# Kernel optimization log

Hardware: AMD Instinct MI355X
Metric: run time of the kernel (lower is better)

Reference implementation:

```python
import jax, jax.numpy as jnp
import numpy as np

P = 16          # patch_len
EPS = 1e-5      # BatchNorm eps


def _dct_mats(L):
    # torch_dct DCT-II matrices. Do: norm='ortho' (orthonormal). D2: norm=None (2*cos).
    n = np.arange(L)
    C = np.cos(np.pi * (n[None, :] + 0.5) * n[:, None] / L)
    s = np.full(L, np.sqrt(2.0 / L)); s[0] = np.sqrt(1.0 / L)
    Do = (s[:, None] * C).astype(np.float32)
    D2 = (2.0 * C).astype(np.float32)
    S = np.full(L, 1.0 / np.sqrt(2.0 * L)); S[0] = 1.0 / (2.0 * np.sqrt(L))
    return jnp.asarray(Do), jnp.asarray(D2), jnp.asarray(S.astype(np.float32))


def _gelu(t):
    return jax.nn.gelu(t, approximate=False)


def _bn(x, g, b, ch_axis=1):
    # training-mode BatchNorm1d: biased batch stats over all axes except channel
    axes = tuple(i for i in range(x.ndim) if i != ch_axis)
    m = x.mean(axes, keepdims=True)
    v = ((x - m) ** 2).mean(axes, keepdims=True)
    shp = [1] * x.ndim; shp[ch_axis] = x.shape[ch_axis]
    return (x - m) / jnp.sqrt(v + EPS) * g.reshape(shp) + b.reshape(shp)


def _quantile(a, q):
    # torch.quantile default 'linear' interpolation over flattened tensor
    s = jnp.sort(a)
    n = a.shape[0]
    pos = q * (n - 1)
    lo = jnp.clip(jnp.floor(pos).astype(jnp.int32), 0, n - 1)
    hi = jnp.clip(lo + 1, 0, n - 1)
    frac = pos - lo.astype(pos.dtype)
    return s[lo] * (1.0 - frac) + s[hi] * frac


def _topk_freq(x, Do5, wf, bf, g, b, wc, bc):
    # TopKFreq: first 5 ortho-DCT coeffs per var (torch detaches via cpu/numpy round trip)
    low = jax.lax.stop_gradient(jnp.einsum('bdl,kl->bdk', x, Do5))  # [B,D,5]
    att = jnp.einsum('bdk,k->bd', low, wf) + bf                      # conv1d k=5 stride=5
    m = att.mean(); v = ((att - m) ** 2).mean()                      # BatchNorm1d(1)
    att = (att - m) / jnp.sqrt(v + EPS) * g + b
    att = _gelu(att)
    a = jax.nn.sigmoid(att * wc + bc)                                # 1x1 conv + sigmoid
    return a[:, :, None]  # [B,D,1]; att1 == att2 (same conv used twice)


def _forward(x, dctconv_w, dctconv_b, dctnorm_g, dctnorm_b, threshold,
             embed_W, embed_b, linres_W, linres_b, depth1_w, depth1_b,
             depthnorm_g, depthnorm_b, tf_fc_w, tf_fc_b, tf_norm_g, tf_norm_b,
             tf_conv_w, tf_conv_b, mlp_w1, mlp_b1, mlp_w2, mlp_b2,
             mlpnorm_g, mlpnorm_b):
    B, L, D = x.shape
    N = L // P
    Do, D2, S = _dct_mats(L)
    dctconv = lambda t: t * dctconv_w[None, :, None] + dctconv_b[None, :, None]

    xp = x.transpose(0, 2, 1)                      # [B,D,L]
    x_res = dctconv(xp)
    z_dct = xp @ D2.T                              # dct, norm=None

    # adaptive high-freq mask (rows of 0/1 per (b,d))
    energy = (z_dct ** 2).sum(-1)                  # [B,D]
    med = jnp.median(energy, axis=1, keepdims=True)
    ne = energy / (med + 1e-6)
    thr = _quantile(ne.ravel(), threshold[0])
    mask = (ne > thr).astype(x.dtype)[:, :, None]

    z = dctconv(z_dct * mask)
    z = _gelu(z)
    z = _bn(z, dctnorm_g, dctnorm_b)
    z1 = (z * S) @ Do + x_res                      # idct(norm=None)

    # non-overlapping patching (stride == patch_len)
    zp = xp.reshape(B * D, N, P)
    ze = jnp.einsum('bnp,dp->bnd', zp, embed_W) + embed_b    # [BD,N,3P]
    z_res = ze.reshape(B, D, N * 3 * P) @ linres_W.T + linres_b  # [B,D,pred]

    zr = ze.reshape(B * D, N, P, 3)                # depthwise conv k=3 stride=3
    z1r = jnp.einsum('bnpj,nj->bnp', zr, depth1_w) + depth1_b[None, :, None]
    zd = _gelu(_bn(z1r, depthnorm_g, depthnorm_b))
    z2 = zd.reshape(B, D, L)

    tf = lambda t: _topk_freq(t, Do[:5], tf_fc_w, tf_fc_b[0], tf_norm_g[0],
                              tf_norm_b[0], tf_conv_w[0], tf_conv_b[0])
    att = tf(z1 + z2)
    z1 = z1 * att
    z2 = z2 * att
    z = z1 + z2
    z_att = tf(z)
    z = _gelu(_bn(z, dctnorm_g, dctnorm_b))
    inter = _gelu(_bn(dctconv(z), dctnorm_g, dctnorm_b)) * z_att
    z1 = z1 * inter + z2
    z2 = z2 * inter + z1                           # uses updated z1
    z = z1 * z2 + z1 + z2
    z = _gelu(_bn(z, dctnorm_g, dctnorm_b))

    # Mlp: fc1 applied twice (identical), gelu gate, BN over vars channel, fc2
    h = z @ mlp_w1.T + mlp_b1                      # [B,D,pred//2]
    h = _gelu(h) * h
    h = _bn(h, mlpnorm_g, mlpnorm_b)
    z_mlp = h @ mlp_w2.T + mlp_b2 + z_res          # [B,D,pred]
    return z_mlp.transpose(0, 2, 1)                # [B,pred,D]


def setup_inputs():
    key = jax.random.key(0)
    ks = jax.random.split(key, 14)
    B, L, D, PRED = 2048, 512, 7, 96
    N, DM, H = L // P, 3 * P, PRED // 2
    f32 = jnp.float32
    rn = lambda k, shape, s: jax.random.normal(k, shape, dtype=f32) * s
    return {
        'x': jax.random.normal(ks[0], (B, L, D), dtype=f32),
        'dctconv_w': rn(ks[1], (D,), 0.5),
        'dctconv_b': rn(ks[2], (D,), 0.02),
        'dctnorm_g': jnp.ones((D,), f32),
        'dctnorm_b': jnp.zeros((D,), f32),
        'threshold': jax.random.uniform(ks[3], (1,), dtype=f32) * 0.5,
        'embed_W': rn(ks[4], (DM, P), 0.1),
        'embed_b': rn(ks[5], (DM,), 0.02),
        'linres_W': rn(ks[6], (PRED, N * DM), 0.02),
        'linres_b': rn(ks[7], (PRED,), 0.02),
        'depth1_w': rn(ks[8], (N, 3), 0.3),
        'depth1_b': rn(ks[9], (N,), 0.02),
        'depthnorm_g': jnp.ones((N,), f32),
        'depthnorm_b': jnp.zeros((N,), f32),
        'tf_fc_w': rn(ks[10], (5,), 0.3),
        'tf_fc_b': rn(ks[10], (1,), 0.02),
        'tf_norm_g': jnp.ones((1,), f32),
        'tf_norm_b': jnp.zeros((1,), f32),
        'tf_conv_w': rn(ks[11], (1,), 0.5),
        'tf_conv_b': rn(ks[11], (1,), 0.02),
        'mlp_w1': rn(ks[12], (H, L), 0.04),
        'mlp_b1': rn(ks[12], (H,), 0.02),
        'mlp_w2': rn(ks[13], (PRED, H), 0.1),
        'mlp_b2': rn(ks[13], (PRED,), 0.02),
        'mlpnorm_g': jnp.ones((D,), f32),
        'mlpnorm_b': jnp.zeros((D,), f32),
    }


def reference(x, dctconv_w, dctconv_b, dctnorm_g, dctnorm_b, threshold,
              embed_W, embed_b, linres_W, linres_b, depth1_w, depth1_b,
              depthnorm_g, depthnorm_b, tf_fc_w, tf_fc_b, tf_norm_g, tf_norm_b,
              tf_conv_w, tf_conv_b, mlp_w1, mlp_b1, mlp_w2, mlp_b2,
              mlpnorm_g, mlpnorm_b):
    return _forward(x, dctconv_w, dctconv_b, dctnorm_g, dctnorm_b, threshold,
                    embed_W, embed_b, linres_W, linres_b, depth1_w, depth1_b,
                    depthnorm_g, depthnorm_b, tf_fc_w, tf_fc_b, tf_norm_g,
                    tf_norm_b, tf_conv_w, tf_conv_b, mlp_w1, mlp_b1, mlp_w2,
                    mlp_b2, mlpnorm_g, mlpnorm_b)
```

## Files before the change

kernel.cpp:

```cpp
#include <hip/hip_runtime.h>
#include <math.h>

#define BB 2048
#define LL 512
#define DD 7
#define BD 14336

constexpr size_t F_XP   = 0;
constexpr size_t F_ZG   = F_XP  + (size_t)BD*512;
constexpr size_t F_Z1   = F_ZG  + (size_t)BD*512;
constexpr size_t F_CLK  = F_Z1  + (size_t)BD*512;
constexpr size_t F_MKL  = F_CLK + 512*512;
constexpr size_t F_U    = F_MKL + 512*512;
constexpr size_t F_CSUM = F_U + 512;
constexpr size_t F_W2   = F_CSUM + 512;
constexpr size_t F_CST  = F_W2 + 96*512;
constexpr size_t F_V    = F_CST + 96;
constexpr size_t F_C2   = F_V + 32*256;
constexpr size_t F_ZRES = F_C2 + 512;
constexpr size_t F_H2   = F_ZRES + (size_t)BD*96;
constexpr size_t F_EN   = F_H2 + (size_t)BD*48;
constexpr size_t F_NE   = F_EN + BD;
constexpr size_t F_ATT  = F_NE + BD;
constexpr size_t F_A1   = F_ATT + BD;
constexpr size_t F_A2   = F_A1 + BD;
constexpr size_t F_RS   = F_A2 + BD;
constexpr size_t F_RQ   = F_RS + BD;
constexpr size_t F_PS   = F_RQ + BD;
constexpr size_t F_PQ   = F_PS + 1792*32;
constexpr size_t F_BN   = F_PQ + 1792*32;
constexpr size_t F_THR  = F_BN + 256;

typedef __attribute__((ext_vector_type(8))) short bf8;
typedef __attribute__((ext_vector_type(4))) float f4;

__device__ __forceinline__ float gelu_f(float x) {
  return 0.5f * x * (1.0f + erff(x * 0.70710678118654752440f));
}
__device__ __forceinline__ float sigm_f(float x) {
  return 1.0f / (1.0f + expf(-x));
}
__device__ __forceinline__ float wred(float v) {
#pragma unroll
  for (int o = 32; o > 0; o >>= 1) v += __shfl_down(v, o);
  return v;
}
__device__ __forceinline__ unsigned bfh_u(float v) {
  unsigned u = __float_as_uint(v);
  return (u + 0x7FFFu + ((u >> 16) & 1u)) >> 16;
}
__device__ __forceinline__ float bf2f(unsigned h) { return __uint_as_float(h << 16); }

__global__ void k_gen_b(ushort* __restrict__ B1H, ushort* __restrict__ B1L,
                        ushort* __restrict__ B2H, ushort* __restrict__ B2L) {
  int c = blockIdx.x;
  for (int r = threadIdx.x; r < 512; r += 256) {
    double c1 = cos(3.14159265358979323846 * (r + 0.5) * c / 512.0);
    float v1 = (float)(2.0 * c1);
    unsigned h = bfh_u(v1);
    B1H[(size_t)c*512 + r] = (ushort)h;
    B1L[(size_t)c*512 + r] = (ushort)bfh_u(v1 - bf2f(h));
    double c2 = cos(3.14159265358979323846 * (c + 0.5) * r / 512.0);
    float v2 = (float)(c2 * (r == 0 ? (1.0/1024.0) : (1.0/512.0)));
    h = bfh_u(v2);
    B2H[(size_t)c*512 + r] = (ushort)h;
    B2L[(size_t)c*512 + r] = (ushort)bfh_u(v2 - bf2f(h));
  }
}

__global__ void k_ucsum2(float* __restrict__ u, float* __restrict__ csum,
                         const float* __restrict__ wf) {
  int l = blockIdx.x*256 + threadIdx.x;
  if (l >= 512) return;
  double th2 = 3.14159265358979323846 * (double)(2*l + 1) / 2048.0;
  double s = (l & 1) ? -1.0 : 1.0;
  double S = 0.5*s/tan(th2) - 0.5;
  csum[l] = (float)(1.0/1024.0 + S/512.0);
  double uu = (double)wf[0] * 45.25483399593904156 / 1024.0;
  for (int k = 1; k < 5; ++k)
    uu += (double)wf[k] * 32.0 * cos(3.14159265358979323846*(l+0.5)*k/512.0) / 512.0;
  u[l] = (float)uu;
}

__global__ __launch_bounds__(256) void k_w2(const float* __restrict__ linW,
    const float* __restrict__ linb, const float* __restrict__ eW, const float* __restrict__ eb,
    ushort* __restrict__ W2H, ushort* __restrict__ W2L, float* __restrict__ cst)
{
  __shared__ float sW[768];
  __shared__ float sb[48];
  __shared__ float rbuf[256];
  int o = blockIdx.x, t = threadIdx.x;
  for (int i = t; i < 768; i += 256) sW[i] = eW[i];
  if (t < 48) sb[t] = eb[t];
  __syncthreads();
  const float* lw = linW + (size_t)o * 1536;
  for (int i = t; i < 512; i += 256) {
    int n = i >> 4, p = i & 15;
    float s = 0.f;
    const float* l2 = lw + n*48;
#pragma unroll 8
    for (int m = 0; m < 48; ++m) s += l2[m] * sW[m*16 + p];
    unsigned hb = bfh_u(s);
    W2H[(size_t)o*512 + i] = (ushort)hb;
    W2L[(size_t)o*512 + i] = (ushort)bfh_u(s - bf2f(hb));
  }
  float c = 0.f;
  for (int i = t; i < 1536; i += 256) c += lw[i] * sb[i % 48];
  rbuf[t] = c; __syncthreads();
  for (int off = 128; off > 0; off >>= 1) { if (t < off) rbuf[t] += rbuf[t+off]; __syncthreads(); }
  if (t == 0) cst[o] = rbuf[0] + linb[o];
}

__global__ void k_splitw(const float* __restrict__ src, ushort* __restrict__ H,
                         ushort* __restrict__ L, int n) {
  int i = blockIdx.x*256 + threadIdx.x;
  if (i < n) {
    float v = src[i];
    unsigned hb = bfh_u(v);
    H[i] = (ushort)hb;
    L[i] = (ushort)bfh_u(v - bf2f(hb));
  }
}

__global__ void k_v(const float* __restrict__ eW, const float* __restrict__ eb,
                    const float* __restrict__ dw, const float* __restrict__ db,
                    float* __restrict__ V, float* __restrict__ c2)
{
  int n = blockIdx.x, t = threadIdx.x;
  int p = t >> 4, q = t & 15;
  float s = 0.f;
#pragma unroll
  for (int j = 0; j < 3; ++j) s += eW[(p*3+j)*16 + q] * dw[n*3+j];
  V[(size_t)n*256 + p*16 + q] = s;
  if (q == 0) {
    float c = 0.f;
#pragma unroll
    for (int j = 0; j < 3; ++j) c += eb[p*3+j] * dw[n*3+j];
    c2[n*16+p] = c + db[n];
  }
}

__global__ __launch_bounds__(256) void k_transpose(const float* __restrict__ x, float* __restrict__ xp) {
  __shared__ float s[3584];
  int b = blockIdx.x;
  const float* src = x + (size_t)b*3584;
  for (int c = threadIdx.x; c < 896; c += 256) {
    float4 v = *(const float4*)&src[c*4];
    s[c*4+0]=v.x; s[c*4+1]=v.y; s[c*4+2]=v.z; s[c*4+3]=v.w;
  }
  __syncthreads();
  for (int c = threadIdx.x; c < 896; c += 256) {
    int d = c >> 7, cg = c & 127;
    float4 v;
    v.x = s[(cg*4+0)*7 + d]; v.y = s[(cg*4+1)*7 + d];
    v.z = s[(cg*4+2)*7 + d]; v.w = s[(cg*4+3)*7 + d];
    *(float4*)&xp[((size_t)b*7 + d)*512 + cg*4] = v;
  }
}

template<int MODE>
__global__ __launch_bounds__(256) void k_mfma(
    const float* __restrict__ Af32,
    const ushort* __restrict__ AHg, const ushort* __restrict__ ALg,
    const ushort* __restrict__ BHg, const ushort* __restrict__ BLg,
    float* __restrict__ z1out, ushort* __restrict__ GH, ushort* __restrict__ GL,
    const float* __restrict__ bnac, const float* __restrict__ csum,
    const float* __restrict__ xp,
    const float* __restrict__ cw, const float* __restrict__ cb,
    const float* __restrict__ ne, const float* __restrict__ thr,
    float* __restrict__ rs, float* __restrict__ rq)
{
  __shared__ ushort AhS[64*40], AlS[64*40];
  __shared__ ushort BhS[256*40], BlS[256*40];
  const int t = threadIdx.x;
  const int lane = t & 63, w = t >> 6;
  const int l15 = lane & 15, l4 = lane >> 4;
  const int r0 = blockIdx.x * 64, c0 = blockIdx.y * 256;

  f4 acc[4][4];
#pragma unroll
  for (int i = 0; i < 4; ++i)
#pragma unroll
    for (int j = 0; j < 4; ++j) acc[i][j] = (f4){0.f,0.f,0.f,0.f};

  const int arow = t >> 2, ak0 = (t & 3) * 8;

  for (int kt = 0; kt < 512; kt += 32) {
    if (MODE == 2) {
      const float* src = Af32 + (size_t)(r0+arow)*512 + kt + ak0;
      float4 v0 = *(const float4*)src;
      float4 v1 = *(const float4*)(src+4);
      float va[8] = {v0.x,v0.y,v0.z,v0.w,v1.x,v1.y,v1.z,v1.w};
      bf8 hv, lv;
#pragma unroll
      for (int j = 0; j < 8; ++j) {
        unsigned hb = bfh_u(va[j]);
        hv[j] = (short)hb;
        lv[j] = (short)bfh_u(va[j] - bf2f(hb));
      }
      *(bf8*)&AhS[arow*40 + ak0] = hv;
      *(bf8*)&AlS[arow*40 + ak0] = lv;
    } else {
      *(bf8*)&AhS[arow*40 + ak0] = *(const bf8*)&AHg[(size_t)(r0+arow)*512 + kt + ak0];
      *(bf8*)&AlS[arow*40 + ak0] = *(const bf8*)&ALg[(size_t)(r0+arow)*512 + kt + ak0];
    }
#pragma unroll
    for (int h = 0; h < 4; ++h) {
      int c = t + h*256;
      int brow = c >> 2, bk0 = (c & 3) * 8;
      *(bf8*)&BhS[brow*40 + bk0] = *(const bf8*)&BHg[(size_t)(c0+brow)*512 + kt + bk0];
      *(bf8*)&BlS[brow*40 + bk0] = *(const bf8*)&BLg[(size_t)(c0+brow)*512 + kt + bk0];
    }
    __syncthreads();
    bf8 ah[4], al[4], bh[4], bl[4];
#pragma unroll
    for (int fr = 0; fr < 4; ++fr) {
      int off = (fr*16 + l15)*40 + l4*8;
      ah[fr] = *(const bf8*)&AhS[off];
      al[fr] = *(const bf8*)&AlS[off];
    }
#pragma unroll
    for (int fc = 0; fc < 4; ++fc) {
      int off = (w*64 + fc*16 + l15)*40 + l4*8;
      bh[fc] = *(const bf8*)&BhS[off];
      bl[fc] = *(const bf8*)&BlS[off];
    }
#pragma unroll
    for (int fr = 0; fr < 4; ++fr)
#pragma unroll
      for (int fc = 0; fc < 4; ++fc) {
        acc[fr][fc] = __builtin_amdgcn_mfma_f32_16x16x32_bf16(ah[fr], bh[fc], acc[fr][fc], 0, 0, 0);
        acc[fr][fc] = __builtin_amdgcn_mfma_f32_16x16x32_bf16(ah[fr], bl[fc], acc[fr][fc], 0, 0, 0);
        acc[fr][fc] = __builtin_amdgcn_mfma_f32_16x16x32_bf16(al[fr], bh[fc], acc[fr][fc], 0, 0, 0);
      }
    __syncthreads();
  }

  const float thv = (MODE == 2) ? thr[0] : 0.f;
#pragma unroll
  for (int fr = 0; fr < 4; ++fr)
#pragma unroll
    for (int j = 0; j < 4; ++j) {
      const int r = r0 + fr*16 + l4*4 + j;
      const int d = r % 7;
      if (MODE == 1) {
        const float aR = bnac[d], cR = bnac[7+d], wv = cw[d], bvv = cb[d];
#pragma unroll
        for (int fc = 0; fc < 4; ++fc) {
          int col = c0 + w*64 + fc*16 + l15;
          float val = acc[fr][fc][j];
          z1out[(size_t)r*512 + col] = aR*val + cR*csum[col] + xp[(size_t)r*512 + col]*wv + bvv;
        }
      } else {
        float m = (ne[r] > thv) ? 1.0f : 0.0f;
        float wm = cw[d] * m, bvv = cb[d];
        float s = 0.f, q = 0.f;
#pragma unroll
        for (int fc = 0; fc < 4; ++fc) {
          int col = c0 + w*64 + fc*16 + l15;
          float g = gelu_f(acc[fr][fc][j]*wm + bvv);
          unsigned hb = bfh_u(g);
          GH[(size_t)r*512 + col] = (ushort)hb;
          GL[(size_t)r*512 + col] = (ushort)bfh_u(g - bf2f(hb));
          s += g; q += g*g;
        }
#pragma unroll
        for (int off = 8; off > 0; off >>= 1) {
          s += __shfl_down(s, off, 16);
          q += __shfl_down(q, off, 16);
        }
        if (l15 == 0) { atomicAdd(&rs[r], s); atomicAdd(&rq[r], q); }
      }
    }
}

template<int NCOLS, int MODE>
__global__ __launch_bounds__(256) void k_mfma_nt(
    const float* __restrict__ Af32,
    const ushort* __restrict__ WH, const ushort* __restrict__ WL,
    const float* __restrict__ bias, float* __restrict__ outp,
    const float* __restrict__ ta, const float* __restrict__ tc,
    float* __restrict__ rs, float* __restrict__ rq)
{
  constexpr int NF = NCOLS / 16;
  __shared__ ushort AhS[64*40], AlS[64*40];
  __shared__ ushort BhS[NCOLS*40], BlS[NCOLS*40];
  const int t = threadIdx.x;
  const int lane = t & 63, w = t >> 6;
  const int l15 = lane & 15, l4 = lane >> 4;
  const int r0 = blockIdx.x * 64;

  f4 acc[NF];
#pragma unroll
  for (int fc = 0; fc < NF; ++fc) acc[fc] = (f4){0.f,0.f,0.f,0.f};

  const int arow = t >> 2, ak0 = (t & 3) * 8;
  float taa = 0.f, tcc = 0.f;
  if (MODE == 1) { int d = (r0 + arow) % 7; taa = ta[d]; tcc = tc[d]; }

  for (int kt = 0; kt < 512; kt += 32) {
    {
      const float* src = Af32 + (size_t)(r0+arow)*512 + kt + ak0;
      float4 v0 = *(const float4*)src;
      float4 v1 = *(const float4*)(src+4);
      float va[8] = {v0.x,v0.y,v0.z,v0.w,v1.x,v1.y,v1.z,v1.w};
      bf8 hv, lv;
#pragma unroll
      for (int j = 0; j < 8; ++j) {
        float x = va[j];
        if (MODE == 1) x = gelu_f(taa*x + tcc);
        unsigned hb = bfh_u(x);
        hv[j] = (short)hb;
        lv[j] = (short)bfh_u(x - bf2f(hb));
      }
      *(bf8*)&AhS[arow*40 + ak0] = hv;
      *(bf8*)&AlS[arow*40 + ak0] = lv;
    }
    for (int c = t; c < NCOLS*4; c += 256) {
      int brow = c >> 2, bk0 = (c & 3) * 8;
      *(bf8*)&BhS[brow*40 + bk0] = *(const bf8*)&WH[(size_t)brow*512 + kt + bk0];
      *(bf8*)&BlS[brow*40 + bk0] = *(const bf8*)&WL[(size_t)brow*512 + kt + bk0];
    }
    __syncthreads();
    bf8 ah, al;
    {
      int off = (w*16 + l15)*40 + l4*8;
      ah = *(const bf8*)&AhS[off];
      al = *(const bf8*)&AlS[off];
    }
#pragma unroll
    for (int fc = 0; fc < NF; ++fc) {
      int off = (fc*16 + l15)*40 + l4*8;
      bf8 bh = *(const bf8*)&BhS[off];
      bf8 bl = *(const bf8*)&BlS[off];
      acc[fc] = __builtin_amdgcn_mfma_f32_16x16x32_bf16(ah, bh, acc[fc], 0, 0, 0);
      acc[fc] = __builtin_amdgcn_mfma_f32_16x16x32_bf16(ah, bl, acc[fc], 0, 0, 0);
      acc[fc] = __builtin_amdgcn_mfma_f32_16x16x32_bf16(al, bh, acc[fc], 0, 0, 0);
    }
    __syncthreads();
  }

#pragma unroll
  for (int j = 0; j < 4; ++j) {
    const int r = r0 + w*16 + l4*4 + j;
    float s = 0.f, q = 0.f;
#pragma unroll
    for (int fc = 0; fc < NF; ++fc) {
      int col = fc*16 + l15;
      float v = acc[fc][j] + bias[col];
      if (MODE == 1) { float g = gelu_f(v); v = g*v; }
      outp[(size_t)r*NCOLS + col] = v;
      if (MODE == 1) { s += v; q += v*v; }
    }
    if (MODE == 1) {
#pragma unroll
      for (int off = 8; off > 0; off >>= 1) {
        s += __shfl_down(s, off, 16);
        q += __shfl_down(q, off, 16);
      }
      if (l15 == 0) { rs[r] = s; rq[r] = q; }
    }
  }
}

__global__ void k_energy_an(const float* __restrict__ xp, float* __restrict__ en) {
  int r = blockIdx.x*4 + (threadIdx.x >> 6);
  int lane = threadIdx.x & 63;
  const float* row = xp + (size_t)r*512;
  double s = 0.0, q = 0.0;
  for (int i = lane; i < 512; i += 64) { double v = row[i]; s += v; q += v*v; }
#pragma unroll
  for (int o = 32; o > 0; o >>= 1) { s += __shfl_down(s, o); q += __shfl_down(q, o); }
  if (lane == 0) en[r] = (float)(1024.0*q + 2.0*s*s);
}

__global__ void k_ne(const float* __restrict__ en, float* __restrict__ ne) {
  int b = blockIdx.x*256 + threadIdx.x;
  if (b >= 2048) return;
  float e[7], s7[7];
#pragma unroll
  for (int d = 0; d < 7; ++d) { e[d] = en[b*7+d]; s7[d] = e[d]; }
#pragma unroll
  for (int i = 1; i < 7; ++i) {
    float key = s7[i]; int j = i-1;
    while (j >= 0 && s7[j] > key) { s7[j+1] = s7[j]; --j; }
    s7[j+1] = key;
  }
  float med = s7[3] + 1e-6f;
#pragma unroll
  for (int d = 0; d < 7; ++d) ne[b*7+d] = e[d] / med;
}

__global__ __launch_bounds__(1024) void k_thr(const float* __restrict__ ne,
                                              const float* __restrict__ qp, float* __restrict__ out)
{
  __shared__ unsigned s_part[16][8];
  __shared__ unsigned s_bsel, s_R;
  const int t = threadIdx.x;
  const int lane = t & 63, wv = t >> 6;
  unsigned key[14];
#pragma unroll
  for (int j = 0; j < 14; ++j) key[j] = __float_as_uint(ne[t + j*1024]);

  float q = qp[0];
  float pos = q * 14335.0f;
  int lo = (int)floorf(pos);
  if (lo < 0) lo = 0; if (lo > 14335) lo = 14335;
  int hi = lo + 1; if (hi > 14335) hi = 14335;
  float frac = pos - (float)lo;

  unsigned prefix = 0;
  unsigned R = (unsigned)lo;
#pragma unroll 1
  for (int shift = 28; shift >= 0; shift -= 4) {
    unsigned pb = prefix >> shift;
    unsigned long long accb = 0ull;
#pragma unroll
    for (int j = 0; j < 14; ++j) {
      unsigned diff = (key[j] >> shift) - pb;
      accb += (diff < 16u) ? (1ull << (diff*4)) : 0ull;
    }
    unsigned pk[8];
#pragma unroll
    for (int b = 0; b < 8; ++b) {
      unsigned clo = (unsigned)(accb >> (b*4)) & 15u;
      unsigned chi = (unsigned)(accb >> (b*4+32)) & 15u;
      pk[b] = clo | (chi << 16);
    }
#pragma unroll
    for (int b = 0; b < 8; ++b)
#pragma unroll
      for (int o = 32; o > 0; o >>= 1) pk[b] += __shfl_down(pk[b], o);
    if (lane == 0) {
#pragma unroll
      for (int b = 0; b < 8; ++b) s_part[wv][b] = pk[b];
    }
    __syncthreads();
    if (t == 0) {
      unsigned tot[16];
#pragma unroll
      for (int i = 0; i < 8; ++i) {
        unsigned s = 0;
#pragma unroll
        for (int w2 = 0; w2 < 16; ++w2) s += s_part[w2][i];
        tot[i] = s & 0xFFFFu; tot[i+8] = s >> 16;
      }
      unsigned cum = 0, bsel = 15;
#pragma unroll 1
      for (int b = 0; b < 16; ++b) {
        if (cum + tot[b] > R) { bsel = (unsigned)b; break; }
        cum += tot[b];
      }
      s_bsel = bsel; s_R = R - cum;
    }
    __syncthreads();
    prefix |= (s_bsel << shift);
    R = s_R;
    __syncthreads();
  }
  unsigned cle = 0, mn = 0xFFFFFFFFu;
#pragma unroll
  for (int j = 0; j < 14; ++j) {
    cle += (key[j] <= prefix) ? 1u : 0u;
    if (key[j] > prefix && key[j] < mn) mn = key[j];
  }
#pragma unroll
  for (int o = 32; o > 0; o >>= 1) {
    cle += __shfl_down(cle, o);
    unsigned m2 = __shfl_down(mn, o);
    mn = (m2 < mn) ? m2 : mn;
  }
  if (lane == 0) { s_part[wv][0] = cle; s_part[wv][1] = mn; }
  __syncthreads();
  if (t == 0) {
    unsigned C = 0, M = 0xFFFFFFFFu;
#pragma unroll
    for (int w2 = 0; w2 < 16; ++w2) {
      C += s_part[w2][0];
      if (s_part[w2][1] < M) M = s_part[w2][1];
    }
    unsigned vhiKey = (C > (unsigned)hi) ? prefix : M;
    if (vhiKey == 0xFFFFFFFFu) vhiKey = prefix;
    float vlo = __uint_as_float(prefix);
    float vhi = __uint_as_float(vhiKey);
    out[0] = vlo*(1.0f-frac) + vhi*frac;
  }
}

__global__ __launch_bounds__(256) void k_bnfin_rows(const float* __restrict__ rs,
    const float* __restrict__ rq, int nch, int nrows, double count,
    const float* __restrict__ gamma, const float* __restrict__ beta, float* __restrict__ out)
{
  __shared__ double sd[256];
  int ch = blockIdx.x, t = threadIdx.x;
  double s = 0.0, q = 0.0;
  for (int i = ch + t*nch; i < nrows; i += 256*nch) { s += rs[i]; q += rq[i]; }
  sd[t] = s; __syncthreads();
  for (int o = 128; o > 0; o >>= 1) { if (t < o) sd[t] += sd[t+o]; __syncthreads(); }
  double S = sd[0]; __syncthreads();
  sd[t] = q; __syncthreads();
  for (int o = 128; o > 0; o >>= 1) { if (t < o) sd[t] += sd[t+o]; __syncthreads(); }
  if (t == 0) {
    double m = S / count;
    double v = sd[0] / count - m*m; if (v < 0.0) v = 0.0;
    double inv = 1.0 / sqrt(v + 1e-5);
    out[ch]       = (float)(gamma[ch] * inv);
    out[nch + ch] = (float)(beta[ch] - m * gamma[ch] * inv);
  }
}

__global__ __launch_bounds__(256) void k_bnfin_part(const float* __restrict__ pS,
    const float* __restrict__ pQ, int nparts, int nch, double count,
    const float* __restrict__ gamma, const float* __restrict__ beta, float* __restrict__ out)
{
  __shared__ double sd[256];
  int ch = blockIdx.x, t = threadIdx.x;
  double s = 0.0, q = 0.0;
  for (int i = t; i < nparts; i += 256) { s += pS[(size_t)i*nch + ch]; q += pQ[(size_t)i*nch + ch]; }
  sd[t] = s; __syncthreads();
  for (int o = 128; o > 0; o >>= 1) { if (t < o) sd[t] += sd[t+o]; __syncthreads(); }
  double S = sd[0]; __syncthreads();
  sd[t] = q; __syncthreads();
  for (int o = 128; o > 0; o >>= 1) { if (t < o) sd[t] += sd[t+o]; __syncthreads(); }
  if (t == 0) {
    double m = S / count;
    double v = sd[0] / count - m*m; if (v < 0.0) v = 0.0;
    double inv = 1.0 / sqrt(v + 1e-5);
    out[ch]       = (float)(gamma[ch] * inv);
    out[nch + ch] = (float)(beta[ch] - m * gamma[ch] * inv);
  }
}

__global__ __launch_bounds__(256) void k_patch(const float* __restrict__ xp,
    const float* __restrict__ V, const float* __restrict__ c2,
    float* __restrict__ z1r, float* __restrict__ pS, float* __restrict__ pQ)
{
  __shared__ float sx[8][512];
  __shared__ float aS[32], aQ[32];
  int t = threadIdx.x;
  int r0 = blockIdx.x * 8;
  for (int c = t; c < 1024; c += 256) {
    int row = c >> 7, cg = c & 127;
    *(float4*)&sx[row][cg*4] = *(const float4*)&xp[(size_t)(r0+row)*512 + cg*4];
  }
  if (t < 32) { aS[t] = 0.f; aQ[t] = 0.f; }
  __syncthreads();
  float vreg[2][16]; float cc[2]; int nn_[2], oo[2];
#pragma unroll
  for (int h = 0; h < 2; ++h) {
    int o = t + h*256;
    oo[h] = o;
    int n = o >> 4, p = o & 15;
    nn_[h] = n;
#pragma unroll
    for (int qg = 0; qg < 4; ++qg) {
      float4 v4 = *(const float4*)&V[(size_t)n*256 + p*16 + qg*4];
      vreg[h][qg*4+0]=v4.x; vreg[h][qg*4+1]=v4.y; vreg[h][qg*4+2]=v4.z; vreg[h][qg*4+3]=v4.w;
    }
    cc[h] = c2[o];
  }
  float sum[2] = {0.f,0.f}, sq[2] = {0.f,0.f};
  for (int row = 0; row < 8; ++row) {
#pragma unroll
    for (int h = 0; h < 2; ++h) {
      const float* xr = &sx[row][nn_[h]*16];
      float val = cc[h];
#pragma unroll
      for (int qq = 0; qq < 16; ++qq) val += vreg[h][qq] * xr[qq];
      z1r[(size_t)(r0+row)*512 + oo[h]] = val;
      sum[h] += val; sq[h] += val*val;
    }
  }
#pragma unroll
  for (int h = 0; h < 2; ++h) {
    atomicAdd(&aS[nn_[h]], sum[h]);
    atomicAdd(&aQ[nn_[h]], sq[h]);
  }
  __syncthreads();
  if (t < 32) { pS[(size_t)blockIdx.x*32 + t] = aS[t]; pQ[(size_t)blockIdx.x*32 + t] = aQ[t]; }
}

__global__ void k_att(const float* __restrict__ z1, const float* __restrict__ z1r,
    const float* __restrict__ bn2, const float* __restrict__ u, const float* __restrict__ fcb,
    float* __restrict__ att)
{
  int r = blockIdx.x*4 + (threadIdx.x >> 6);
  int lane = threadIdx.x & 63;
  const float* z1p = z1 + (size_t)r*512;
  const float* zrp = z1r + (size_t)r*512;
  float s = 0.f;
#pragma unroll
  for (int h = 0; h < 2; ++h) {
    int i = lane*4 + h*256;
    int n = i >> 4;
    float a2n = bn2[n], c2n = bn2[32+n];
    float4 zr = *(const float4*)&zrp[i];
    float4 zv = *(const float4*)&z1p[i];
    float4 uv = *(const float4*)&u[i];
    s += (zv.x + gelu_f(a2n*zr.x + c2n)) * uv.x;
    s += (zv.y + gelu_f(a2n*zr.y + c2n)) * uv.y;
    s += (zv.z + gelu_f(a2n*zr.z + c2n)) * uv.z;
    s += (zv.w + gelu_f(a2n*zr.w + c2n)) * uv.w;
  }
  s = wred(s);
  if (lane == 0) att[r] = s + fcb[0];
}

__global__ __launch_bounds__(1024) void k_tf(const float* __restrict__ att,
    const float* __restrict__ pg, const float* __restrict__ pb,
    const float* __restrict__ pwc, const float* __restrict__ pbc,
    const float* __restrict__ pfb, float* __restrict__ a1, float* __restrict__ a2)
{
  __shared__ double sd[1024];
  __shared__ float sh[4];
  const int t = threadIdx.x;
  float g = pg[0], b = pb[0], wc = pwc[0], bc = pbc[0], fb = pfb[0];
  double s = 0.0, q = 0.0;
  for (int i = t; i < BD; i += 1024) { double v = att[i]; s += v; q += v*v; }
  sd[t] = s; __syncthreads();
  for (int o = 512; o > 0; o >>= 1) { if (t < o) sd[t] += sd[t+o]; __syncthreads(); }
  double S1 = sd[0]; __syncthreads();
  sd[t] = q; __syncthreads();
  for (int o = 512; o > 0; o >>= 1) { if (t < o) sd[t] += sd[t+o]; __syncthreads(); }
  if (t == 0) {
    double m = S1 / 14336.0;
    double v = sd[0] / 14336.0 - m*m; if (v < 0.0) v = 0.0;
    sh[0] = (float)m; sh[1] = (float)(1.0 / sqrt(v + 1e-5));
  }
  __syncthreads();
  float m1 = sh[0], i1 = sh[1];
  s = 0.0; q = 0.0;
  for (int i = t; i < BD; i += 1024) {
    float v = att[i];
    float an = (v - m1) * i1 * g + b;
    float av = sigm_f(gelu_f(an) * wc + bc);
    a1[i] = av;
    float t2 = av * (v - fb) + fb;
    s += t2; q += (double)t2 * t2;
  }
  __syncthreads();
  sd[t] = s; __syncthreads();
  for (int o = 512; o > 0; o >>= 1) { if (t < o) sd[t] += sd[t+o]; __syncthreads(); }
  double S2 = sd[0]; __syncthreads();
  sd[t] = q; __syncthreads();
  for (int o = 512; o > 0; o >>= 1) { if (t < o) sd[t] += sd[t+o]; __syncthreads(); }
  if (t == 0) {
    double m = S2 / 14336.0;
    double v = sd[0] / 14336.0 - m*m; if (v < 0.0) v = 0.0;
    sh[2] = (float)m; sh[3] = (float)(1.0 / sqrt(v + 1e-5));
  }
  __syncthreads();
  float m2 = sh[2], i2 = sh[3];
  for (int i = t; i < BD; i += 1024) {
    float t2 = a1[i] * (att[i] - fb) + fb;
    float an = (t2 - m2) * i2 * g + b;
    a2[i] = sigm_f(gelu_f(an) * wc + bc);
  }
}

__global__ void k_statsA(const float* __restrict__ z1, const float* __restrict__ z1r,
    const float* __restrict__ bn2, const float* __restrict__ a1,
    float* __restrict__ rs, float* __restrict__ rq)
{
  int r = blockIdx.x*4 + (threadIdx.x >> 6);
  int lane = threadIdx.x & 63;
  float av = a1[r];
  const float* z1p = z1 + (size_t)r*512;
  const float* zrp = z1r + (size_t)r*512;
  float s = 0.f, q = 0.f;
#pragma unroll
  for (int h = 0; h < 2; ++h) {
    int i = lane*4 + h*256;
    int n = i >> 4;
    float a2n = bn2[n], c2n = bn2[32+n];
    float4 zr = *(const float4*)&zrp[i];
    float4 zv = *(const float4*)&z1p[i];
    float A0 = (zv.x + gelu_f(a2n*zr.x + c2n)) * av;
    float A1 = (zv.y + gelu_f(a2n*zr.y + c2n)) * av;
    float A2 = (zv.z + gelu_f(a2n*zr.z + c2n)) * av;
    float A3 = (zv.w + gelu_f(a2n*zr.w + c2n)) * av;
    s += A0+A1+A2+A3; q += A0*A0+A1*A1+A2*A2+A3*A3;
  }
  s = wred(s); q = wred(q);
  if (lane == 0) { rs[r] = s; rq[r] = q; }
}

__global__ void k_statsC(const float* __restrict__ z1, const float* __restrict__ z1r,
    const float* __restrict__ bn2, const float* __restrict__ a1,
    const float* __restrict__ bn3, const float* __restrict__ cw, const float* __restrict__ cb,
    float* __restrict__ rs, float* __restrict__ rq)
{
  int r = blockIdx.x*4 + (threadIdx.x >> 6);
  int lane = threadIdx.x & 63;
  int d = r % 7;
  float av = a1[r];
  float b3a = bn3[d], b3c = bn3[7+d], wv = cw[d], bv = cb[d];
  const float* z1p = z1 + (size_t)r*512;
  const float* zrp = z1r + (size_t)r*512;
  float s = 0.f, q = 0.f;
#pragma unroll
  for (int h = 0; h < 2; ++h) {
    int i = lane*4 + h*256;
    int n = i >> 4;
    float a2n = bn2[n], c2n = bn2[32+n];
    float4 zr = *(const float4*)&zrp[i];
    float4 zv = *(const float4*)&z1p[i];
#pragma unroll
    for (int e = 0; e < 4; ++e) {
      float ze = (e==0?zr.x:e==1?zr.y:e==2?zr.z:zr.w);
      float z1e = (e==0?zv.x:e==1?zv.y:e==2?zv.z:zv.w);
      float A = (z1e + gelu_f(a2n*ze + c2n)) * av;
      float C = wv*gelu_f(b3a*A + b3c) + bv;
      s += C; q += C*C;
    }
  }
  s = wred(s); q = wred(q);
  if (lane == 0) { rs[r] = s; rq[r] = q; }
}

__global__ void k_final(const float* __restrict__ z1, const float* __restrict__ z1r,
    const float* __restrict__ bn2, const float* __restrict__ a1, const float* __restrict__ a2,
    const float* __restrict__ bn3, const float* __restrict__ bn4,
    const float* __restrict__ cw, const float* __restrict__ cb,
    float* __restrict__ zf, float* __restrict__ rs, float* __restrict__ rq)
{
  int r = blockIdx.x*4 + (threadIdx.x >> 6);
  int lane = threadIdx.x & 63;
  int d = r % 7;
  float av = a1[r], a2v = a2[r];
  float b3a = bn3[d], b3c = bn3[7+d], b4a = bn4[d], b4c = bn4[7+d];
  float wv = cw[d], bv = cb[d];
  const float* z1p = z1 + (size_t)r*512;
  const float* zrp = z1r + (size_t)r*512;
  float* zfp = zf + (size_t)r*512;
  float s = 0.f, q = 0.f;
#pragma unroll
  for (int h = 0; h < 2; ++h) {
    int i = lane*4 + h*256;
    int n = i >> 4;
    float a2n = bn2[n], c2n = bn2[32+n];
    float4 zr = *(const float4*)&zrp[i];
    float4 zv = *(const float4*)&z1p[i];
    float4 ov;
#pragma unroll
    for (int e = 0; e < 4; ++e) {
      float ze = (e==0?zr.x:e==1?zr.y:e==2?zr.z:zr.w);
      float z1e = (e==0?zv.x:e==1?zv.y:e==2?zv.z:zv.w);
      float z1v = z1e * av;
      float z2v = gelu_f(a2n*ze + c2n) * av;
      float A = z1v + z2v;
      float C = wv*gelu_f(b3a*A + b3c) + bv;
      float inter = gelu_f(b4a*C + b4c) * a2v;
      float z1n = z1v*inter + z2v;
      float z2n = z2v*inter + z1n;
      float zfv = z1n*z2n + z1n + z2n;
      (e==0?ov.x:e==1?ov.y:e==2?ov.z:ov.w) = zfv;
      s += zfv; q += zfv*zfv;
    }
    *(float4*)&zfp[i] = ov;
  }
  s = wred(s); q = wred(q);
  if (lane == 0) { rs[r] = s; rq[r] = q; }
}

__global__ __launch_bounds__(256) void k_out(const float* __restrict__ h2,
    const float* __restrict__ bn6, const float* __restrict__ w2, const float* __restrict__ b2,
    const float* __restrict__ zres, float* __restrict__ out)
{
  int idx = blockIdx.x*256 + threadIdx.x;
  int r = idx / 96, o = idx - r*96;
  int d = r % 7, b = r / 7;
  float a6 = bn6[d], c6 = bn6[7+d];
  const float* hp = h2 + (size_t)r*48;
  const float* wp = w2 + o*48;
  float s = 0.f;
#pragma unroll
  for (int j4 = 0; j4 < 12; ++j4) {
    float4 hv = *(const float4*)&hp[j4*4];
    float4 wv = *(const float4*)&wp[j4*4];
    s += (a6*hv.x + c6)*wv.x + (a6*hv.y + c6)*wv.y
       + (a6*hv.z + c6)*wv.z + (a6*hv.w + c6)*wv.w;
  }
  out[(size_t)b*672 + o*7 + d] = s + b2[o] + zres[(size_t)r*96 + o];
}

extern "C" void kernel_launch(void* const* d_in, const int* in_sizes, int n_in,
                              void* d_out, int out_size, void* d_ws, size_t ws_size,
                              hipStream_t stream) {
  const float* x          = (const float*)d_in[0];
  const float* dctconv_w  = (const float*)d_in[1];
  const float* dctconv_b  = (const float*)d_in[2];
  const float* dctnorm_g  = (const float*)d_in[3];
  const float* dctnorm_b  = (const float*)d_in[4];
  const float* threshold  = (const float*)d_in[5];
  const float* embed_W    = (const float*)d_in[6];
  const float* embed_b    = (const float*)d_in[7];
  const float* linres_W   = (const float*)d_in[8];
  const float* linres_b   = (const float*)d_in[9];
  const float* depth1_w   = (const float*)d_in[10];
  const float* depth1_b   = (const float*)d_in[11];
  const float* depthnorm_g= (const float*)d_in[12];
  const float* depthnorm_b= (const float*)d_in[13];
  const float* tf_fc_w    = (const float*)d_in[14];
  const float* tf_fc_b    = (const float*)d_in[15];
  const float* tf_norm_g  = (const float*)d_in[16];
  const float* tf_norm_b  = (const float*)d_in[17];
  const float* tf_conv_w  = (const float*)d_in[18];
  const float* tf_conv_b  = (const float*)d_in[19];
  const float* mlp_w1     = (const float*)d_in[20];
  const float* mlp_b1     = (const float*)d_in[21];
  const float* mlp_w2     = (const float*)d_in[22];
  const float* mlp_b2     = (const float*)d_in[23];
  const float* mlpnorm_g  = (const float*)d_in[24];
  const float* mlpnorm_b  = (const float*)d_in[25];
  float* out = (float*)d_out;
  float* ws  = (float*)d_ws;

  float* XP   = ws + F_XP;
  float* ZG   = ws + F_ZG;
  ushort* ZGH = (ushort*)(ws + F_ZG);
  ushort* ZGL = ZGH + (size_t)BD*512;
  float* Z1   = ws + F_Z1;
  ushort* B1H = (ushort*)(ws + F_CLK);
  ushort* B1L = B1H + 512*512;
  ushort* W2H = (ushort*)(ws + F_CLK + 131072);
  ushort* W2L = W2H + 96*512;
  ushort* W1H = W2L + 96*512;
  ushort* W1L = W1H + 48*512;
  ushort* B2H = (ushort*)(ws + F_MKL);
  ushort* B2L = B2H + 512*512;
  float* U    = ws + F_U;
  float* CSUM = ws + F_CSUM;
  float* CSTp = ws + F_CST;
  float* Vp   = ws + F_V;
  float* C2p  = ws + F_C2;
  float* ZRES = ws + F_ZRES;
  float* H2p  = ws + F_H2;
  float* EN   = ws + F_EN;
  float* NEp  = ws + F_NE;
  float* ATTp = ws + F_ATT;
  float* A1p  = ws + F_A1;
  float* A2p  = ws + F_A2;
  float* RS   = ws + F_RS;
  float* RQ   = ws + F_RQ;
  float* PS   = ws + F_PS;
  float* PQ   = ws + F_PQ;
  float* BN0  = ws + F_BN;
  float* BN2  = ws + F_BN + 16;
  float* BN3  = ws + F_BN + 80;
  float* BN4  = ws + F_BN + 96;
  float* BN5  = ws + F_BN + 112;
  float* BN6  = ws + F_BN + 128;
  float* THRp = ws + F_THR;

  k_gen_b<<<512, 256, 0, stream>>>(B1H, B1L, B2H, B2L);
  k_ucsum2<<<2, 256, 0, stream>>>(U, CSUM, tf_fc_w);
  k_w2<<<96, 256, 0, stream>>>(linres_W, linres_b, embed_W, embed_b, W2H, W2L, CSTp);
  k_splitw<<<96, 256, 0, stream>>>(mlp_w1, W1H, W1L, 48*512);
  k_v<<<32, 256, 0, stream>>>(embed_W, embed_b, depth1_w, depth1_b, Vp, C2p);
  k_transpose<<<2048, 256, 0, stream>>>(x, XP);
  k_energy_an<<<3584, 256, 0, stream>>>(XP, EN);
  k_ne<<<8, 256, 0, stream>>>(EN, NEp);
  k_thr<<<1, 1024, 0, stream>>>(NEp, threshold, THRp);
  hipMemsetAsync(RS, 0, 2*BD*sizeof(float), stream);
  k_mfma<2><<<dim3(224,2), 256, 0, stream>>>(XP, nullptr, nullptr, B1H, B1L,
      nullptr, ZGH, ZGL, nullptr, nullptr, nullptr, dctconv_w, dctconv_b,
      NEp, THRp, RS, RQ);
  k_bnfin_rows<<<7, 256, 0, stream>>>(RS, RQ, 7, BD, 1048576.0, dctnorm_g, dctnorm_b, BN0);
  k_mfma<1><<<dim3(224,2), 256, 0, stream>>>(nullptr, ZGH, ZGL, B2H, B2L,
      Z1, nullptr, nullptr, BN0, CSUM, XP, dctconv_w, dctconv_b,
      nullptr, nullptr, nullptr, nullptr);
  k_patch<<<1792, 256, 0, stream>>>(XP, Vp, C2p, ZG, PS, PQ);
  k_bnfin_part<<<32, 256, 0, stream>>>(PS, PQ, 1792, 32, 229376.0, depthnorm_g, depthnorm_b, BN2);
  k_mfma_nt<96,0><<<224, 256, 0, stream>>>(XP, W2H, W2L, CSTp, ZRES,
      nullptr, nullptr, nullptr, nullptr);
  k_att<<<3584, 256, 0, stream>>>(Z1, ZG, BN2, U, tf_fc_b, ATTp);
  k_tf<<<1, 1024, 0, stream>>>(ATTp, tf_norm_g, tf_norm_b, tf_conv_w, tf_conv_b, tf_fc_b, A1p, A2p);
  k_statsA<<<3584, 256, 0, stream>>>(Z1, ZG, BN2, A1p, RS, RQ);
  k_bnfin_rows<<<7, 256, 0, stream>>>(RS, RQ, 7, BD, 1048576.0, dctnorm_g, dctnorm_b, BN3);
  k_statsC<<<3584, 256, 0, stream>>>(Z1, ZG, BN2, A1p, BN3, dctconv_w, dctconv_b, RS, RQ);
  k_bnfin_rows<<<7, 256, 0, stream>>>(RS, RQ, 7, BD, 1048576.0, dctnorm_g, dctnorm_b, BN4);
  k_final<<<3584, 256, 0, stream>>>(Z1, ZG, BN2, A1p, A2p, BN3, BN4, dctconv_w, dctconv_b, XP, RS, RQ);
  k_bnfin_rows<<<7, 256, 0, stream>>>(RS, RQ, 7, BD, 1048576.0, dctnorm_g, dctnorm_b, BN5);
  k_mfma_nt<48,1><<<224, 256, 0, stream>>>(XP, W1H, W1L, mlp_b1, H2p,
      BN5, BN5+7, RS, RQ);
  k_bnfin_rows<<<7, 256, 0, stream>>>(RS, RQ, 7, BD, 98304.0, mlpnorm_g, mlpnorm_b, BN6);
  k_out<<<5376, 256, 0, stream>>>(H2p, BN6, mlp_w2, mlp_b2, ZRES, out);
}
```

Baseline: 385.7 us.

## Fuse energy computation into transpose and use 8-wave blocks for MFMA GEMMs

```diff
diff --git a/kernel.cpp b/kernel.cpp
--- a/kernel.cpp
+++ b/kernel.cpp
@@ -32,6 +32,7 @@
 constexpr size_t F_THR  = F_BN + 256;
 
 typedef __attribute__((ext_vector_type(8))) short bf8;
+typedef __attribute__((ext_vector_type(4))) short sh4;
 typedef __attribute__((ext_vector_type(4))) float f4;
 
 __device__ __forceinline__ float gelu_f(float x) {
@@ -140,7 +141,9 @@
   }
 }
 
-__global__ __launch_bounds__(256) void k_transpose(const float* __restrict__ x, float* __restrict__ xp) {
+__global__ __launch_bounds__(256) void k_transpose(const float* __restrict__ x,
+                                                   float* __restrict__ xp,
+                                                   float* __restrict__ en) {
   __shared__ float s[3584];
   int b = blockIdx.x;
   const float* src = x + (size_t)b*3584;
@@ -156,10 +159,25 @@
     v.z = s[(cg*4+2)*7 + d]; v.w = s[(cg*4+3)*7 + d];
     *(float4*)&xp[((size_t)b*7 + d)*512 + cg*4] = v;
   }
+  int t = threadIdx.x;
+  if (t < 224) {
+    int d = t >> 5, c0 = (t & 31) * 16;
+    double ss = 0.0, qq = 0.0;
+    for (int l = c0; l < c0 + 16; ++l) {
+      double v = s[l*7 + d];
+      ss += v; qq += v*v;
+    }
+#pragma unroll
+    for (int o = 16; o > 0; o >>= 1) {
+      ss += __shfl_down(ss, o, 32);
+      qq += __shfl_down(qq, o, 32);
+    }
+    if ((t & 31) == 0) en[b*7 + d] = (float)(1024.0*qq + 2.0*ss*ss);
+  }
 }
 
 template<int MODE>
-__global__ __launch_bounds__(256) void k_mfma(
+__global__ __launch_bounds__(512) void k_mfma(
     const float* __restrict__ Af32,
     const ushort* __restrict__ AHg, const ushort* __restrict__ ALg,
     const ushort* __restrict__ BHg, const ushort* __restrict__ BLg,
@@ -175,58 +193,58 @@
   const int t = threadIdx.x;
   const int lane = t & 63, w = t >> 6;
   const int l15 = lane & 15, l4 = lane >> 4;
+  const int rg = w & 1, cg = w >> 1;
   const int r0 = blockIdx.x * 64, c0 = blockIdx.y * 256;
 
-  f4 acc[4][4];
-#pragma unroll
-  for (int i = 0; i < 4; ++i)
+  f4 acc[2][4];
+#pragma unroll
+  for (int i = 0; i < 2; ++i)
 #pragma unroll
     for (int j = 0; j < 4; ++j) acc[i][j] = (f4){0.f,0.f,0.f,0.f};
 
-  const int arow = t >> 2, ak0 = (t & 3) * 8;
+  const int arow = t >> 3, ak0 = (t & 7) * 4;
 
   for (int kt = 0; kt < 512; kt += 32) {
     if (MODE == 2) {
       const float* src = Af32 + (size_t)(r0+arow)*512 + kt + ak0;
       float4 v0 = *(const float4*)src;
-      float4 v1 = *(const float4*)(src+4);
-      float va[8] = {v0.x,v0.y,v0.z,v0.w,v1.x,v1.y,v1.z,v1.w};
-      bf8 hv, lv;
-#pragma unroll
-      for (int j = 0; j < 8; ++j) {
+      float va[4] = {v0.x,v0.y,v0.z,v0.w};
+      sh4 hv, lv;
+#pragma unroll
+      for (int j = 0; j < 4; ++j) {
         unsigned hb = bfh_u(va[j]);
         hv[j] = (short)hb;
         lv[j] = (short)bfh_u(va[j] - bf2f(hb));
       }
-      *(bf8*)&AhS[arow*40 + ak0] = hv;
-      *(bf8*)&AlS[arow*40 + ak0] = lv;
+      *(sh4*)&AhS[arow*40 + ak0] = hv;
+      *(sh4*)&AlS[arow*40 + ak0] = lv;
     } else {
-      *(bf8*)&AhS[arow*40 + ak0] = *(const bf8*)&AHg[(size_t)(r0+arow)*512 + kt + ak0];
-      *(bf8*)&AlS[arow*40 + ak0] = *(const bf8*)&ALg[(size_t)(r0+arow)*512 + kt + ak0];
-    }
-#pragma unroll
-    for (int h = 0; h < 4; ++h) {
-      int c = t + h*256;
+      *(sh4*)&AhS[arow*40 + ak0] = *(const sh4*)&AHg[(size_t)(r0+arow)*512 + kt + ak0];
+      *(sh4*)&AlS[arow*40 + ak0] = *(const sh4*)&ALg[(size_t)(r0+arow)*512 + kt + ak0];
+    }
+#pragma unroll
+    for (int h = 0; h < 2; ++h) {
+      int c = t + h*512;
       int brow = c >> 2, bk0 = (c & 3) * 8;
       *(bf8*)&BhS[brow*40 + bk0] = *(const bf8*)&BHg[(size_t)(c0+brow)*512 + kt + bk0];
       *(bf8*)&BlS[brow*40 + bk0] = *(const bf8*)&BLg[(size_t)(c0+brow)*512 + kt + bk0];
     }
     __syncthreads();
-    bf8 ah[4], al[4], bh[4], bl[4];
-#pragma unroll
-    for (int fr = 0; fr < 4; ++fr) {
-      int off = (fr*16 + l15)*40 + l4*8;
+    bf8 ah[2], al[2], bh[4], bl[4];
+#pragma unroll
+    for (int fr = 0; fr < 2; ++fr) {
+      int off = (rg*32 + fr*16 + l15)*40 + l4*8;
       ah[fr] = *(const bf8*)&AhS[off];
       al[fr] = *(const bf8*)&AlS[off];
     }
 #pragma unroll
     for (int fc = 0; fc < 4; ++fc) {
-      int off = (w*64 + fc*16 + l15)*40 + l4*8;
+      int off = (cg*64 + fc*16 + l15)*40 + l4*8;
       bh[fc] = *(const bf8*)&BhS[off];
       bl[fc] = *(const bf8*)&BlS[off];
     }
 #pragma unroll
-    for (int fr = 0; fr < 4; ++fr)
+    for (int fr = 0; fr < 2; ++fr)
 #pragma unroll
       for (int fc = 0; fc < 4; ++fc) {
         acc[fr][fc] = __builtin_amdgcn_mfma_f32_16x16x32_bf16(ah[fr], bh[fc], acc[fr][fc], 0, 0, 0);
@@ -238,16 +256,16 @@
 
   const float thv = (MODE == 2) ? thr[0] : 0.f;
 #pragma unroll
-  for (int fr = 0; fr < 4; ++fr)
+  for (int fr = 0; fr < 2; ++fr)
 #pragma unroll
     for (int j = 0; j < 4; ++j) {
-      const int r = r0 + fr*16 + l4*4 + j;
+      const int r = r0 + rg*32 + fr*16 + l4*4 + j;
       const int d = r % 7;
       if (MODE == 1) {
         const float aR = bnac[d], cR = bnac[7+d], wv = cw[d], bvv = cb[d];
 #pragma unroll
         for (int fc = 0; fc < 4; ++fc) {
-          int col = c0 + w*64 + fc*16 + l15;
+          int col = c0 + cg*64 + fc*16 + l15;
           float val = acc[fr][fc][j];
           z1out[(size_t)r*512 + col] = aR*val + cR*csum[col] + xp[(size_t)r*512 + col]*wv + bvv;
         }
@@ -257,7 +275,7 @@
         float s = 0.f, q = 0.f;
 #pragma unroll
         for (int fc = 0; fc < 4; ++fc) {
-          int col = c0 + w*64 + fc*16 + l15;
+          int col = c0 + cg*64 + fc*16 + l15;
           float g = gelu_f(acc[fr][fc][j]*wm + bvv);
           unsigned hb = bfh_u(g);
           GH[(size_t)r*512 + col] = (ushort)hb;
@@ -361,17 +379,6 @@
       if (l15 == 0) { rs[r] = s; rq[r] = q; }
     }
   }
-}
-
-__global__ void k_energy_an(const float* __restrict__ xp, float* __restrict__ en) {
-  int r = blockIdx.x*4 + (threadIdx.x >> 6);
-  int lane = threadIdx.x & 63;
-  const float* row = xp + (size_t)r*512;
-  double s = 0.0, q = 0.0;
-  for (int i = lane; i < 512; i += 64) { double v = row[i]; s += v; q += v*v; }
-#pragma unroll
-  for (int o = 32; o > 0; o >>= 1) { s += __shfl_down(s, o); q += __shfl_down(q, o); }
-  if (lane == 0) en[r] = (float)(1024.0*q + 2.0*s*s);
 }
 
 __global__ void k_ne(const float* __restrict__ en, float* __restrict__ ne) {
@@ -858,16 +865,15 @@
   k_w2<<<96, 256, 0, stream>>>(linres_W, linres_b, embed_W, embed_b, W2H, W2L, CSTp);
   k_splitw<<<96, 256, 0, stream>>>(mlp_w1, W1H, W1L, 48*512);
   k_v<<<32, 256, 0, stream>>>(embed_W, embed_b, depth1_w, depth1_b, Vp, C2p);
-  k_transpose<<<2048, 256, 0, stream>>>(x, XP);
-  k_energy_an<<<3584, 256, 0, stream>>>(XP, EN);
+  k_transpose<<<2048, 256, 0, stream>>>(x, XP, EN);
   k_ne<<<8, 256, 0, stream>>>(EN, NEp);
   k_thr<<<1, 1024, 0, stream>>>(NEp, threshold, THRp);
   hipMemsetAsync(RS, 0, 2*BD*sizeof(float), stream);
-  k_mfma<2><<<dim3(224,2), 256, 0, stream>>>(XP, nullptr, nullptr, B1H, B1L,
+  k_mfma<2><<<dim3(224,2), 512, 0, stream>>>(XP, nullptr, nullptr, B1H, B1L,
       nullptr, ZGH, ZGL, nullptr, nullptr, nullptr, dctconv_w, dctconv_b,
       NEp, THRp, RS, RQ);
   k_bnfin_rows<<<7, 256, 0, stream>>>(RS, RQ, 7, BD, 1048576.0, dctnorm_g, dctnorm_b, BN0);
-  k_mfma<1><<<dim3(224,2), 256, 0, stream>>>(nullptr, ZGH, ZGL, B2H, B2L,
+  k_mfma<1><<<dim3(224,2), 512, 0, stream>>>(nullptr, ZGH, ZGL, B2H, B2L,
       Z1, nullptr, nullptr, BN0, CSUM, XP, dctconv_w, dctconv_b,
       nullptr, nullptr, nullptr, nullptr);
   k_patch<<<1792, 256, 0, stream>>>(XP, Vp, C2p, ZG, PS, PQ);
```

Result: no change. 379.8 us (-1.5%).
